# Performance work log

Measured on AMD Instinct MI355X. Metric: run time of the kernel, lower is better.

## Reference

```python
import jax, jax.numpy as jnp
import numpy as np

N, E, DIN, DH, DOUT, H, G = 50000, 640000, 128, 64, 64, 4, 16

_PARAM_SHAPES = {
    "gat1_W": (DIN, H * DH), "gat1_asrc": (H, DH), "gat1_adst": (H, DH), "gat1_b": (DH,),
    "gat2_W": (DH, H * DH), "gat2_asrc": (H, DH), "gat2_adst": (H, DH), "gat2_b": (DH,),
    "gin_W1": (DH, DH), "gin_b1": (DH,), "gin_W2": (DH, DH), "gin_b2": (DH,),
    "sage1_Wl": (DH, DH), "sage1_bl": (DH,), "sage1_Wr": (DH, DH),
    "sage2_Wl": (DH, DH), "sage2_bl": (DH,), "sage2_Wr": (DH, DH),
    "tr_Wq": (DH, H * DH), "tr_bq": (H * DH,), "tr_Wk": (DH, H * DH), "tr_bk": (H * DH,),
    "tr_Wv": (DH, H * DH), "tr_bv": (H * DH,), "tr_Ws": (DH, DH), "tr_bs": (DH,),
    "ec_W1": (2 * DH, DH), "ec_b1": (DH,), "ec_W2": (DH, DH), "ec_b2": (DH,),
    "fc1_W": (DH, DH), "fc1_b": (DH,), "fc2_W": (DH, DOUT), "fc2_b": (DOUT,),
}
_PARAM_NAMES = list(_PARAM_SHAPES)


def setup_inputs() -> dict:
    key = jax.random.key(0)
    inp = {}
    inp["x"] = jax.random.normal(jax.random.fold_in(key, 0), (N, DIN), jnp.float32)
    inp["edge_index"] = jax.random.randint(jax.random.fold_in(key, 1), (2, E), 0, N, dtype=jnp.int32)
    inp["batch"] = jnp.sort(jax.random.randint(jax.random.fold_in(key, 2), (N,), 0, G, dtype=jnp.int32))
    for i, (name, shp) in enumerate(_PARAM_SHAPES.items()):
        inp[name] = jax.random.normal(jax.random.fold_in(key, 10 + i), shp, jnp.float32) * 0.05
    return inp


def _edge_softmax(logit, dst, n):
    # softmax over incoming edges of each target node (PyG scatter-softmax)
    m = jax.ops.segment_max(logit, dst, num_segments=n)
    e = jnp.exp(logit - m[dst])
    z = jax.ops.segment_sum(e, dst, num_segments=n)
    return e / (z[dst] + 1e-16)


def _forward(x, src, dst, batch, p):
    relu = jax.nn.relu
    # GATConv adds self-loops by default
    loop = jnp.arange(N, dtype=src.dtype)
    src_sl = jnp.concatenate([src, loop])
    dst_sl = jnp.concatenate([dst, loop])

    def gat(h_in, W, a_s, a_d, b):
        h = (h_in @ W).reshape(N, H, DH)                    # [N,H,D]
        ls = jnp.einsum('nhd,hd->nh', h, a_s)
        ld = jnp.einsum('nhd,hd->nh', h, a_d)
        logit = jax.nn.leaky_relu(ls[src_sl] + ld[dst_sl], 0.2)   # [E+N,H]
        alpha = _edge_softmax(logit, dst_sl, N)
        out = jax.ops.segment_sum(h[src_sl] * alpha[:, :, None], dst_sl, num_segments=N)
        return out.mean(axis=1) + b                          # concat=False -> head mean + bias

    x1 = relu(gat(x, p["gat1_W"], p["gat1_asrc"], p["gat1_adst"], p["gat1_b"]))
    x2 = relu(gat(x1, p["gat2_W"], p["gat2_asrc"], p["gat2_adst"], p["gat2_b"]))

    # GINConv: nn((1+eps)*x + sum_j x_j), eps=0
    agg = jax.ops.segment_sum(x2[src], dst, num_segments=N)
    x3 = relu(relu((x2 + agg) @ p["gin_W1"] + p["gin_b1"]) @ p["gin_W2"] + p["gin_b2"])

    deg = jax.ops.segment_sum(jnp.ones((E,), x.dtype), dst, num_segments=N)
    deg = jnp.maximum(deg, 1.0)[:, None]

    def sage(h_in, Wl, bl, Wr):
        mean = jax.ops.segment_sum(h_in[src], dst, num_segments=N) / deg
        return mean @ Wl + bl + h_in @ Wr

    xs = relu(sage(x3, p["sage1_Wl"], p["sage1_bl"], p["sage1_Wr"]))
    x4 = relu(sage(xs, p["sage2_Wl"], p["sage2_bl"], p["sage2_Wr"]))

    # TransformerConv (heads=4, concat=False, root_weight skip)
    q = (x4 @ p["tr_Wq"] + p["tr_bq"]).reshape(N, H, DH)
    k = (x4 @ p["tr_Wk"] + p["tr_bk"]).reshape(N, H, DH)
    v = (x4 @ p["tr_Wv"] + p["tr_bv"]).reshape(N, H, DH)
    logit = (q[dst] * k[src]).sum(-1) * (1.0 / np.sqrt(DH))  # [E,H]
    alpha = _edge_softmax(logit, dst, N)
    tout = jax.ops.segment_sum(v[src] * alpha[:, :, None], dst, num_segments=N).mean(axis=1)
    x5 = relu(tout + x4 @ p["tr_Ws"] + p["tr_bs"])

    # EdgeConv: max_j nn([x_i, x_j - x_i])
    xi = x5[dst]
    feat = jnp.concatenate([xi, x5[src] - xi], axis=1)       # [E, 2*DH]
    msg = relu(feat @ p["ec_W1"] + p["ec_b1"]) @ p["ec_W2"] + p["ec_b2"]
    emax = jax.ops.segment_max(msg, dst, num_segments=N)
    x6 = relu(jnp.where(jnp.isfinite(emax), emax, 0.0))      # isolated nodes -> 0

    # global_mean_pool over batch ids
    cnt = jax.ops.segment_sum(jnp.ones((N,), x.dtype), batch, num_segments=G)
    gmean = jax.ops.segment_sum(x6, batch, num_segments=G) / jnp.maximum(cnt, 1.0)[:, None]

    # dropout layers are identity in eval mode
    return relu(gmean @ p["fc1_W"] + p["fc1_b"]) @ p["fc2_W"] + p["fc2_b"]


def reference(x, edge_index, batch,
              gat1_W, gat1_asrc, gat1_adst, gat1_b,
              gat2_W, gat2_asrc, gat2_adst, gat2_b,
              gin_W1, gin_b1, gin_W2, gin_b2,
              sage1_Wl, sage1_bl, sage1_Wr,
              sage2_Wl, sage2_bl, sage2_Wr,
              tr_Wq, tr_bq, tr_Wk, tr_bk, tr_Wv, tr_bv, tr_Ws, tr_bs,
              ec_W1, ec_b1, ec_W2, ec_b2,
              fc1_W, fc1_b, fc2_W, fc2_b):
    L = dict(locals())
    p = {n: L[n] for n in _PARAM_NAMES}
    return _forward(x, edge_index[0], edge_index[1], batch, p)
```

## Files before the change

kernel.cpp:

```cpp
#include <hip/hip_runtime.h>

#define NN 50000
#define EE 640000
#define GG 16
#define N64 (NN*64)

static inline int cdiv(int a,int b){return (a+b-1)/b;}

typedef __attribute__((ext_vector_type(8))) short bfrag;
typedef __attribute__((ext_vector_type(4))) float ffrag;

__device__ __forceinline__ float lrelu(float x){ return x>0.f? x : 0.2f*x; }
__device__ __forceinline__ unsigned fenc(float f){
  unsigned u=__float_as_uint(f);
  return (u&0x80000000u)? ~u : (u|0x80000000u);
}
__device__ __forceinline__ float bf2f(unsigned short u){ return __uint_as_float(((unsigned)u)<<16); }
__device__ __forceinline__ unsigned short f2bf(float f){
  unsigned u=__float_as_uint(f);
  u += 0x7FFFu + ((u>>16)&1u);
  return (unsigned short)(u>>16);
}
__device__ __forceinline__ void mac4(float* acc, const float4 av,
    const float4 w0, const float4 w1, const float4 w2, const float4 w3){
  acc[0]+=av.x*w0.x+av.y*w1.x+av.z*w2.x+av.w*w3.x;
  acc[1]+=av.x*w0.y+av.y*w1.y+av.z*w2.y+av.w*w3.y;
  acc[2]+=av.x*w0.z+av.y*w1.z+av.z*w2.z+av.w*w3.z;
  acc[3]+=av.x*w0.w+av.y*w1.w+av.z*w2.w+av.w*w3.w;
}

__global__ void zero_kernel(unsigned* p, int n){
  int i=blockIdx.x*blockDim.x+threadIdx.x;
  if(i<n) p[i]=0u;
}

__global__ void hist_kernel(const int* __restrict__ dst, int* __restrict__ cnt){
  int e=blockIdx.x*blockDim.x+threadIdx.x;
  if(e<EE) atomicAdd(&cnt[dst[e]],1);
}

__global__ __launch_bounds__(1024) void scan1_kernel(const int* __restrict__ cnt,
    int* __restrict__ rowptr, int* __restrict__ bsum){
  __shared__ int wsum[16];
  int t=threadIdx.x, b=blockIdx.x;
  int i=b*1024+t;
  int v=(i<NN)?cnt[i]:0;
  int lane=t&63, w=t>>6;
  int inc=v;
  #pragma unroll
  for(int o=1;o<64;o<<=1){ int u=__shfl_up(inc,o,64); if(lane>=o) inc+=u; }
  if(lane==63) wsum[w]=inc;
  __syncthreads();
  if(t<16){
    int s=wsum[t];
    #pragma unroll
    for(int o=1;o<16;o<<=1){ int u=__shfl_up(s,o,16); if(t>=o) s+=u; }
    wsum[t]=s;
  }
  __syncthreads();
  int woff=(w>0)?wsum[w-1]:0;
  if(i<NN) rowptr[i]=woff+inc-v;
  if(t==1023) bsum[b]=wsum[15];
}

__global__ void scan2_kernel(const int* __restrict__ bsum, int* __restrict__ boff, int* __restrict__ rowptr, int nb){
  int t=threadIdx.x;
  int v=(t<nb)?bsum[t]:0;
  int inc=v;
  #pragma unroll
  for(int o=1;o<64;o<<=1){ int u=__shfl_up(inc,o,64); if(t>=o) inc+=u; }
  if(t<nb) boff[t]=inc-v;
  if(t==63) rowptr[NN]=inc;
}

__global__ void scan3_kernel(int* __restrict__ rowptr, const int* __restrict__ boff,
                             const int* __restrict__ cnt, float* __restrict__ invdeg){
  int i=blockIdx.x*blockDim.x+threadIdx.x;
  if(i<NN){
    rowptr[i]+=boff[i>>10];
    invdeg[i]=1.f/fmaxf((float)cnt[i],1.f);
  }
}

__global__ void fill_kernel(const int* __restrict__ src, const int* __restrict__ dst,
                            const int* __restrict__ rowptr, int* __restrict__ fillp,
                            int* __restrict__ srcS, int* __restrict__ dstS){
  int e=blockIdx.x*blockDim.x+threadIdx.x;
  if(e>=EE) return;
  int d=dst[e];
  int p=rowptr[d]+atomicAdd(&fillp[d],1);
  srcS[p]=src[e]; dstS[p]=d;
}

__global__ void cvtx_kernel(const float* __restrict__ x, unsigned short* __restrict__ xb){
  int i=blockIdx.x*blockDim.x+threadIdx.x;
  if(i>=NN*32) return;
  float4 v=*(const float4*)(x+(size_t)i*4);
  ushort4 o; o.x=f2bf(v.x); o.y=f2bf(v.y); o.z=f2bf(v.z); o.w=f2bf(v.w);
  *(ushort4*)(xb+(size_t)i*4)=o;
}

__global__ void prep_kernel(
    const float* __restrict__ g1W, const float* __restrict__ g2W,
    const float* __restrict__ giW1, const float* __restrict__ giW2,
    const float* __restrict__ s1Wl, const float* __restrict__ s1Wr,
    const float* __restrict__ s2Wl, const float* __restrict__ s2Wr,
    const float* __restrict__ Wq, const float* __restrict__ Wk,
    const float* __restrict__ Wv, const float* __restrict__ Ws,
    const float* __restrict__ ecW1,
    const float* __restrict__ bq, const float* __restrict__ bk, const float* __restrict__ eb1,
    unsigned short* __restrict__ wt, float* __restrict__ bqk, float* __restrict__ bPQ){
  int i=blockIdx.x*blockDim.x+threadIdx.x;
  if(i<32768){ int n=i>>7,k=i&127; wt[i]=f2bf(g1W[k*256+n]); return; } i-=32768;
  if(i<16384){ int n=i>>6,k=i&63; wt[32768+i]=f2bf(g2W[k*256+n]); return; } i-=16384;
  if(i<4096){ int n=i>>6,k=i&63; wt[49152+i]=f2bf(giW1[k*64+n]); return; } i-=4096;
  if(i<4096){ int n=i>>6,k=i&63; wt[53248+i]=f2bf(giW2[k*64+n]); return; } i-=4096;
  if(i<8192){ int n=i>>7,k=i&127; float v=(k<64)?s1Wl[k*64+n]:s1Wr[(k-64)*64+n];
              wt[57344+i]=f2bf(v); return; } i-=8192;
  if(i<8192){ int n=i>>7,k=i&127; float v=(k<64)?s2Wl[k*64+n]:s2Wr[(k-64)*64+n];
              wt[65536+i]=f2bf(v); return; } i-=8192;
  if(i<32768){ int n=i>>6,k=i&63; float v=(n<256)?Wq[k*256+n]:Wk[k*256+(n-256)];
               wt[73728+i]=f2bf(v); return; } i-=32768;
  if(i<16384){ int n=i>>6,k=i&63; wt[106496+i]=f2bf(Wv[k*256+n]); return; } i-=16384;
  if(i<4096){ int n=i>>6,k=i&63; wt[122880+i]=f2bf(Ws[k*64+n]); return; } i-=4096;
  if(i<8192){ int n=i>>6,k=i&63;
              float v=(n<64)?(ecW1[k*64+n]-ecW1[(64+k)*64+n]):ecW1[(64+k)*64+(n-64)];
              wt[126976+i]=f2bf(v); return; } i-=8192;
  if(i<640){
    if(i<256) bqk[i]=bq[i];
    else if(i<512) bqk[i]=bk[i-256];
    else { int j=i-512; bPQ[j]=(j<64)?eb1[j]:0.f; }
  }
}

template<int K>
__global__ __launch_bounds__(256) void mgemm_kernel(
    const unsigned short* __restrict__ A, const unsigned short* __restrict__ Wt,
    const float* __restrict__ bias,
    float* __restrict__ Cf, unsigned short* __restrict__ Cb, int ldc, int relu_flag,
    const float* __restrict__ a_s, const float* __restrict__ a_d,
    float* __restrict__ lsO, float* __restrict__ ldO){
  __shared__ float lsP[2][4][64];
  const int m0=blockIdx.x*64;
  const int tid=threadIdx.x;
  const int w=tid>>6, l=tid&63, lo=l&15, quad=l>>4;
  const int colg=blockIdx.y*64 + w*16 + lo;
  const unsigned short* wrow=Wt+(size_t)colg*K+quad*8;
  ffrag acc[4];
  #pragma unroll
  for(int t=0;t<4;t++) acc[t]=(ffrag){0.f,0.f,0.f,0.f};
  int rows[4];
  #pragma unroll
  for(int t=0;t<4;t++){ int r=m0+t*16+lo; rows[t]=(r<NN)?r:(NN-1); }
  #pragma unroll
  for(int kc=0;kc<K;kc+=32){
    bfrag b=*(const bfrag*)(wrow+kc);
    #pragma unroll
    for(int t=0;t<4;t++){
      bfrag a=*(const bfrag*)(A+(size_t)rows[t]*K+kc+quad*8);
      acc[t]=__builtin_amdgcn_mfma_f32_16x16x32_bf16(a,b,acc[t],0,0,0);
    }
  }
  float bv=bias?bias[colg]:0.f;
  float asv=0.f,adv=0.f;
  if(lsO){ asv=a_s[colg]; adv=a_d[colg]; }
  #pragma unroll
  for(int t=0;t<4;t++){
    #pragma unroll
    for(int r=0;r<4;r++){
      float v=acc[t][r]+bv;
      if(relu_flag) v=fmaxf(v,0.f);
      int row=m0+t*16+quad*4+r;
      if(row<NN){
        if(Cb) Cb[(size_t)row*ldc+colg]=f2bf(v);
        else   Cf[(size_t)row*ldc+colg]=v;
      }
      if(lsO){
        float ps=v*asv, pd=v*adv;
        #pragma unroll
        for(int o=1;o<16;o<<=1){ ps+=__shfl_xor(ps,o,16); pd+=__shfl_xor(pd,o,16); }
        if(lo==0){ int lr=t*16+quad*4+r; lsP[0][w][lr]=ps; lsP[1][w][lr]=pd; }
      }
    }
  }
  if(lsO){
    __syncthreads();
    if(tid<64){
      int row=m0+tid;
      if(row<NN){
        lsO[(size_t)row*4+blockIdx.y]=lsP[0][0][tid]+lsP[0][1][tid]+lsP[0][2][tid]+lsP[0][3][tid];
        ldO[(size_t)row*4+blockIdx.y]=lsP[1][0][tid]+lsP[1][1][tid]+lsP[1][2][tid]+lsP[1][3][tid];
      }
    }
  }
}

__global__ __launch_bounds__(256) void gat1p_kernel(const unsigned short* __restrict__ h,
    const int* __restrict__ rowptr, const int* __restrict__ srcS,
    const float* __restrict__ ls4, const float* __restrict__ ld4,
    const float* __restrict__ bias, unsigned short* __restrict__ outb){
  int n=blockIdx.x*4+(threadIdx.x>>6);
  int lane=threadIdx.x&63;
  if(n>=NN) return;
  int r0=rowptr[n], r1=rowptr[n+1];
  const float4 ldv=*(const float4*)(ld4+(size_t)4*n);
  const float4 lsv=*(const float4*)(ls4+(size_t)4*n);
  float z0=__expf(lrelu(lsv.x+ldv.x)), z1=__expf(lrelu(lsv.y+ldv.y));
  float z2=__expf(lrelu(lsv.z+ldv.z)), z3=__expf(lrelu(lsv.w+ldv.w));
  const unsigned short* hn=h+(size_t)n*256;
  float a0=z0*bf2f(hn[lane]), a1=z1*bf2f(hn[64+lane]), a2=z2*bf2f(hn[128+lane]), a3=z3*bf2f(hn[192+lane]);
  int j=r0;
  for(; j+3<r1; j+=4){
    int s0=srcS[j], s1=srcS[j+1], s2=srcS[j+2], s3=srcS[j+3];
    const float4 A0=*(const float4*)(ls4+(size_t)4*s0);
    const float4 A1=*(const float4*)(ls4+(size_t)4*s1);
    const float4 A2=*(const float4*)(ls4+(size_t)4*s2);
    const float4 A3=*(const float4*)(ls4+(size_t)4*s3);
    const unsigned short* h0=h+(size_t)s0*256;
    const unsigned short* h1=h+(size_t)s1*256;
    const unsigned short* h2=h+(size_t)s2*256;
    const unsigned short* h3=h+(size_t)s3*256;
    float e00=__expf(lrelu(A0.x+ldv.x)), e01=__expf(lrelu(A0.y+ldv.y));
    float e02=__expf(lrelu(A0.z+ldv.z)), e03=__expf(lrelu(A0.w+ldv.w));
    float e10=__expf(lrelu(A1.x+ldv.x)), e11=__expf(lrelu(A1.y+ldv.y));
    float e12=__expf(lrelu(A1.z+ldv.z)), e13=__expf(lrelu(A1.w+ldv.w));
    float e20=__expf(lrelu(A2.x+ldv.x)), e21=__expf(lrelu(A2.y+ldv.y));
    float e22=__expf(lrelu(A2.z+ldv.z)), e23=__expf(lrelu(A2.w+ldv.w));
    float e30=__expf(lrelu(A3.x+ldv.x)), e31=__expf(lrelu(A3.y+ldv.y));
    float e32=__expf(lrelu(A3.z+ldv.z)), e33=__expf(lrelu(A3.w+ldv.w));
    z0+=(e00+e10)+(e20+e30); z1+=(e01+e11)+(e21+e31);
    z2+=(e02+e12)+(e22+e32); z3+=(e03+e13)+(e23+e33);
    a0+=(e00*bf2f(h0[lane])+e10*bf2f(h1[lane]))+(e20*bf2f(h2[lane])+e30*bf2f(h3[lane]));
    a1+=(e01*bf2f(h0[64+lane])+e11*bf2f(h1[64+lane]))+(e21*bf2f(h2[64+lane])+e31*bf2f(h3[64+lane]));
    a2+=(e02*bf2f(h0[128+lane])+e12*bf2f(h1[128+lane]))+(e22*bf2f(h2[128+lane])+e32*bf2f(h3[128+lane]));
    a3+=(e03*bf2f(h0[192+lane])+e13*bf2f(h1[192+lane]))+(e23*bf2f(h2[192+lane])+e33*bf2f(h3[192+lane]));
  }
  for(; j<r1; j++){
    int s0=srcS[j];
    const float4 A0=*(const float4*)(ls4+(size_t)4*s0);
    const unsigned short* h0=h+(size_t)s0*256;
    float e00=__expf(lrelu(A0.x+ldv.x)), e01=__expf(lrelu(A0.y+ldv.y));
    float e02=__expf(lrelu(A0.z+ldv.z)), e03=__expf(lrelu(A0.w+ldv.w));
    z0+=e00; z1+=e01; z2+=e02; z3+=e03;
    a0+=e00*bf2f(h0[lane]); a1+=e01*bf2f(h0[64+lane]); a2+=e02*bf2f(h0[128+lane]); a3+=e03*bf2f(h0[192+lane]);
  }
  float zi0=1.f/(z0+1e-16f), zi1=1.f/(z1+1e-16f), zi2=1.f/(z2+1e-16f), zi3=1.f/(z3+1e-16f);
  float r=fmaxf(0.25f*(a0*zi0+a1*zi1+a2*zi2+a3*zi3)+bias[lane],0.f);
  outb[(size_t)n*64+lane]=f2bf(r);
}

__global__ __launch_bounds__(256) void agg_kernel(const unsigned short* __restrict__ xin,
    const int* __restrict__ rowptr, const int* __restrict__ srcS,
    unsigned short* __restrict__ out){
  int n=blockIdx.x*4+(threadIdx.x>>6);
  int lane=threadIdx.x&63;
  if(n>=NN) return;
  int r0=rowptr[n], r1=rowptr[n+1];
  float acc=bf2f(xin[(size_t)n*64+lane]);
  int j=r0;
  for(; j+3<r1; j+=4){
    int s0=srcS[j], s1=srcS[j+1], s2=srcS[j+2], s3=srcS[j+3];
    acc+=(bf2f(xin[(size_t)s0*64+lane])+bf2f(xin[(size_t)s1*64+lane]))
        +(bf2f(xin[(size_t)s2*64+lane])+bf2f(xin[(size_t)s3*64+lane]));
  }
  for(; j<r1; j++) acc+=bf2f(xin[(size_t)srcS[j]*64+lane]);
  out[(size_t)n*64+lane]=f2bf(acc);
}

__global__ __launch_bounds__(256) void agg2_kernel(const unsigned short* __restrict__ xin,
    const int* __restrict__ rowptr, const int* __restrict__ srcS,
    const float* __restrict__ invdeg, unsigned short* __restrict__ out128b){
  int n=blockIdx.x*4+(threadIdx.x>>6);
  int lane=threadIdx.x&63;
  if(n>=NN) return;
  int r0=rowptr[n], r1=rowptr[n+1];
  float acc=0.f;
  int j=r0;
  for(; j+3<r1; j+=4){
    int s0=srcS[j], s1=srcS[j+1], s2=srcS[j+2], s3=srcS[j+3];
    acc+=(bf2f(xin[(size_t)s0*64+lane])+bf2f(xin[(size_t)s1*64+lane]))
        +(bf2f(xin[(size_t)s2*64+lane])+bf2f(xin[(size_t)s3*64+lane]));
  }
  for(; j<r1; j++) acc+=bf2f(xin[(size_t)srcS[j]*64+lane]);
  out128b[(size_t)n*128+lane]=f2bf(acc*invdeg[n]);
  out128b[(size_t)n*128+64+lane]=xin[(size_t)n*64+lane];
}

__global__ __launch_bounds__(256) void tr_pass1_kernel(const int* __restrict__ srcS, const int* __restrict__ dstS,
    const unsigned short* __restrict__ qk, float* __restrict__ lg){
  int e=blockIdx.x*16+(threadIdx.x>>4);
  int t=threadIdx.x&15;
  if(e>=EE) return;
  int s=srcS[e], d=dstS[e];
  const unsigned short* qd=qk+(size_t)d*512+t*4;
  const unsigned short* ks=qk+(size_t)s*512+256+t*4;
  ushort4 ku0=*(const ushort4*)(ks);
  ushort4 ku1=*(const ushort4*)(ks+64);
  ushort4 ku2=*(const ushort4*)(ks+128);
  ushort4 ku3=*(const ushort4*)(ks+192);
  ushort4 qu0=*(const ushort4*)(qd);
  ushort4 qu1=*(const ushort4*)(qd+64);
  ushort4 qu2=*(const ushort4*)(qd+128);
  ushort4 qu3=*(const ushort4*)(qd+192);
  float v0=bf2f(ku0.x)*bf2f(qu0.x)+bf2f(ku0.y)*bf2f(qu0.y)+bf2f(ku0.z)*bf2f(qu0.z)+bf2f(ku0.w)*bf2f(qu0.w);
  float v1=bf2f(ku1.x)*bf2f(qu1.x)+bf2f(ku1.y)*bf2f(qu1.y)+bf2f(ku1.z)*bf2f(qu1.z)+bf2f(ku1.w)*bf2f(qu1.w);
  float v2=bf2f(ku2.x)*bf2f(qu2.x)+bf2f(ku2.y)*bf2f(qu2.y)+bf2f(ku2.z)*bf2f(qu2.z)+bf2f(ku2.w)*bf2f(qu2.w);
  float v3=bf2f(ku3.x)*bf2f(qu3.x)+bf2f(ku3.y)*bf2f(qu3.y)+bf2f(ku3.z)*bf2f(qu3.z)+bf2f(ku3.w)*bf2f(qu3.w);
  #pragma unroll
  for(int o=1;o<16;o<<=1){
    v0+=__shfl_xor(v0,o,16); v1+=__shfl_xor(v1,o,16);
    v2+=__shfl_xor(v2,o,16); v3+=__shfl_xor(v3,o,16);
  }
  if(t==0)
    *(float4*)(lg+(size_t)4*e)=make_float4(v0*0.125f,v1*0.125f,v2*0.125f,v3*0.125f);
}

__global__ __launch_bounds__(256) void tr_pass2_kernel(const int* __restrict__ rowptr, const int* __restrict__ srcS,
    const float* __restrict__ lg,
    const unsigned short* __restrict__ v, const float* __restrict__ skip, unsigned short* __restrict__ x5b){
  int n=blockIdx.x*4+(threadIdx.x>>6);
  int lane=threadIdx.x&63;
  if(n>=NN) return;
  int r0=rowptr[n], r1=rowptr[n+1];
  float z0=0.f,z1=0.f,z2=0.f,z3=0.f;
  float a0=0.f,a1=0.f,a2=0.f,a3=0.f;
  int j=r0;
  for(; j+3<r1; j+=4){
    int s0=srcS[j], s1=srcS[j+1], s2=srcS[j+2], s3=srcS[j+3];
    const float4 f0=*(const float4*)(lg+(size_t)4*j);
    const float4 f1=*(const float4*)(lg+(size_t)4*(j+1));
    const float4 f2=*(const float4*)(lg+(size_t)4*(j+2));
    const float4 f3=*(const float4*)(lg+(size_t)4*(j+3));
    const unsigned short* v0=v+(size_t)s0*256;
    const unsigned short* v1=v+(size_t)s1*256;
    const unsigned short* v2=v+(size_t)s2*256;
    const unsigned short* v3=v+(size_t)s3*256;
    float e00=__expf(f0.x), e01=__expf(f0.y), e02=__expf(f0.z), e03=__expf(f0.w);
    float e10=__expf(f1.x), e11=__expf(f1.y), e12=__expf(f1.z), e13=__expf(f1.w);
    float e20=__expf(f2.x), e21=__expf(f2.y), e22=__expf(f2.z), e23=__expf(f2.w);
    float e30=__expf(f3.x), e31=__expf(f3.y), e32=__expf(f3.z), e33=__expf(f3.w);
    z0+=(e00+e10)+(e20+e30); z1+=(e01+e11)+(e21+e31);
    z2+=(e02+e12)+(e22+e32); z3+=(e03+e13)+(e23+e33);
    a0+=(e00*bf2f(v0[lane])+e10*bf2f(v1[lane]))+(e20*bf2f(v2[lane])+e30*bf2f(v3[lane]));
    a1+=(e01*bf2f(v0[64+lane])+e11*bf2f(v1[64+lane]))+(e21*bf2f(v2[64+lane])+e31*bf2f(v3[64+lane]));
    a2+=(e02*bf2f(v0[128+lane])+e12*bf2f(v1[128+lane]))+(e22*bf2f(v2[128+lane])+e32*bf2f(v3[128+lane]));
    a3+=(e03*bf2f(v0[192+lane])+e13*bf2f(v1[192+lane]))+(e23*bf2f(v2[192+lane])+e33*bf2f(v3[192+lane]));
  }
  for(; j<r1; j++){
    int s0=srcS[j];
    const float4 f0=*(const float4*)(lg+(size_t)4*j);
    const unsigned short* v0=v+(size_t)s0*256;
    float e00=__expf(f0.x), e01=__expf(f0.y), e02=__expf(f0.z), e03=__expf(f0.w);
    z0+=e00; z1+=e01; z2+=e02; z3+=e03;
    a0+=e00*bf2f(v0[lane]); a1+=e01*bf2f(v0[64+lane]); a2+=e02*bf2f(v0[128+lane]); a3+=e03*bf2f(v0[192+lane]);
  }
  float zi0=1.f/(z0+1e-16f), zi1=1.f/(z1+1e-16f), zi2=1.f/(z2+1e-16f), zi3=1.f/(z3+1e-16f);
  float t=0.25f*(a0*zi0+a1*zi1+a2*zi2+a3*zi3)+skip[(size_t)n*64+lane];
  x5b[(size_t)n*64+lane]=f2bf(fmaxf(t,0.f));
}

__global__ __launch_bounds__(256) void edgeconv2_kernel(
    const float* __restrict__ PQ,
    const int* __restrict__ srcS, const int* __restrict__ dstS,
    const float* __restrict__ W2, const float* __restrict__ b2,
    unsigned* __restrict__ emax){
  __shared__ float As[64][68];
  __shared__ float Ws[64][64];
  __shared__ int dstL[64];
  const int e0=blockIdx.x*64;
  const int tid=threadIdx.x, tx=tid&15, ty=tid>>4;
  if(tid<64) dstL[tid]=dstS[e0+tid];
  #pragma unroll
  for(int it=0;it<4;it++){
    int linear=it*1024+tid*4;
    int m=linear>>6, k=linear&63;
    int e=e0+m;
    int dn=dstS[e], sn=srcS[e];
    const float4 p=*(const float4*)(PQ+(size_t)dn*128+k);
    const float4 q=*(const float4*)(PQ+(size_t)sn*128+64+k);
    float4 v=make_float4(fmaxf(p.x+q.x,0.f),fmaxf(p.y+q.y,0.f),fmaxf(p.z+q.z,0.f),fmaxf(p.w+q.w,0.f));
    *(float4*)&As[m][k]=v;
  }
  #pragma unroll
  for(int it=0;it<4;it++){
    int linear=it*1024+tid*4;
    int k=linear>>6, n=linear&63;
    *(float4*)&Ws[k][n]=*(const float4*)(W2+(size_t)k*64+n);
  }
  __syncthreads();
  float acc2[4][4];
  #pragma unroll
  for(int i=0;i<4;i++)
    #pragma unroll
    for(int j=0;j<4;j++) acc2[i][j]=b2[tx*4+j];
  #pragma unroll 8
  for(int k=0;k<64;k+=4){
    float4 a0=*(float4*)&As[ty*4+0][k];
    float4 a1=*(float4*)&As[ty*4+1][k];
    float4 a2=*(float4*)&As[ty*4+2][k];
    float4 a3=*(float4*)&As[ty*4+3][k];
    float4 w0=*(float4*)&Ws[k+0][tx*4];
    float4 w1=*(float4*)&Ws[k+1][tx*4];
    float4 w2=*(float4*)&Ws[k+2][tx*4];
    float4 w3=*(float4*)&Ws[k+3][tx*4];
    mac4(acc2[0],a0,w0,w1,w2,w3);
    mac4(acc2[1],a1,w0,w1,w2,w3);
    mac4(acc2[2],a2,w0,w1,w2,w3);
    mac4(acc2[3],a3,w0,w1,w2,w3);
  }
  __syncthreads();
  #pragma unroll
  for(int i=0;i<4;i++)
    #pragma unroll
    for(int j=0;j<4;j++)
      As[ty*4+i][tx*4+j]=acc2[i][j];
  __syncthreads();
  if(tid<64){
    const int c=tid;
    const int dFirst=dstL[0], dLast=dstL[63];
    int dprev=dFirst;
    float mx=As[0][c];
    #pragma unroll 8
    for(int m=1;m<64;m++){
      int dn=dstL[m];
      float v=As[m][c];
      if(dn!=dprev){
        unsigned* addr=&emax[(size_t)dprev*64+c];
        unsigned enc=fenc(mx);
        if(dprev!=dFirst && dprev!=dLast) *addr=enc;
        else atomicMax(addr,enc);
        dprev=dn; mx=v;
      }else mx=fmaxf(mx,v);
    }
    unsigned* addr=&emax[(size_t)dprev*64+c];
    unsigned enc=fenc(mx);
    if(dprev!=dFirst && dprev!=dLast) *addr=enc;
    else atomicMax(addr,enc);
  }
}

__global__ __launch_bounds__(256) void pool_kernel(const unsigned* __restrict__ emax, const int* __restrict__ batch,
                                                   float* __restrict__ pooled){
  const int NB=200;
  int base=blockIdx.x*NB;
  int lane=threadIdx.x&63;
  int wsub=threadIdx.x>>6;
  float acc=0.f; int curg=-1;
  for(int idx=wsub; idx<NB; idx+=4){
    int n=base+idx;
    if(n>=NN) break;
    int g=batch[n];
    if(g!=curg){
      if(curg>=0) atomicAdd(&pooled[curg*64+lane],acc);
      acc=0.f; curg=g;
    }
    unsigned u=emax[(size_t)n*64+lane];
    acc+=(u>=0x80000000u)? __uint_as_float(u&0x7fffffffu) : 0.f;
  }
  if(curg>=0) atomicAdd(&pooled[curg*64+lane],acc);
}

__global__ __launch_bounds__(256) void final_kernel(const float* __restrict__ pooled, const int* __restrict__ batch,
    const float* __restrict__ fc1W, const float* __restrict__ fc1b,
    const float* __restrict__ fc2W, const float* __restrict__ fc2b,
    float* __restrict__ out){
  __shared__ float gm[16][64];
  __shared__ float t1[16][64];
  __shared__ int cgs[17];
// ... 33 lines not shown
  const int*   src     =ei;
  const int*   dst     =ei+EE;
  const int*   batch   =(const int*)  d_in[2];
  const float* gat1_W  =(const float*)d_in[3];
  const float* gat1_as =(const float*)d_in[4];
  const float* gat1_ad =(const float*)d_in[5];
  const float* gat1_b  =(const float*)d_in[6];
  const float* gat2_W  =(const float*)d_in[7];
  const float* gat2_as =(const float*)d_in[8];
  const float* gat2_ad =(const float*)d_in[9];
  const float* gat2_b  =(const float*)d_in[10];
  const float* gin_W1  =(const float*)d_in[11];
  const float* gin_b1  =(const float*)d_in[12];
  const float* gin_W2  =(const float*)d_in[13];
  const float* gin_b2  =(const float*)d_in[14];
  const float* sage1_Wl=(const float*)d_in[15];
  const float* sage1_bl=(const float*)d_in[16];
  const float* sage1_Wr=(const float*)d_in[17];
  const float* sage2_Wl=(const float*)d_in[18];
  const float* sage2_bl=(const float*)d_in[19];
  const float* sage2_Wr=(const float*)d_in[20];
  const float* tr_Wq   =(const float*)d_in[21];
  const float* tr_bq   =(const float*)d_in[22];
  const float* tr_Wk   =(const float*)d_in[23];
  const float* tr_bk   =(const float*)d_in[24];
  const float* tr_Wv   =(const float*)d_in[25];
  const float* tr_bv   =(const float*)d_in[26];
  const float* tr_Ws   =(const float*)d_in[27];
  const float* tr_bs   =(const float*)d_in[28];
  const float* ec_W1   =(const float*)d_in[29];
  const float* ec_b1   =(const float*)d_in[30];
  const float* ec_W2   =(const float*)d_in[31];
  const float* ec_b2   =(const float*)d_in[32];
  const float* fc1_W   =(const float*)d_in[33];
  const float* fc1_b   =(const float*)d_in[34];
  const float* fc2_W   =(const float*)d_in[35];
  const float* fc2_b   =(const float*)d_in[36];

  float* base=(float*)d_ws;
  size_t off=0;
  auto alloc=[&](size_t n){ float* p=base+off; off+=n; return p; };
  float* A_big =alloc((size_t)NN*256);
  float* nb0   =alloc(N64);
  float* nb1   =alloc(N64);
  float* nb2   =alloc(N64);
  float* nb3   =alloc(N64);
  float* nb4   =alloc(N64);
  float* nb5   =alloc(N64);
  float* logitE=alloc((size_t)EE*4);
  float* ls    =alloc(NN*4);
  float* ldb   =alloc(NN*4);
  float* invdeg=alloc(NN);
  float* pooled=alloc(GG*64);
  float* wbuf  =alloc(68000);
  float* bbuf  =alloc(640);
  int* ibase=(int*)(base+off);
  int* srcS  =ibase;
  int* dstS  =ibase+EE;
  int* cnt   =ibase+2*EE;
  int* fillp =ibase+2*EE+NN;
  int* rowptr=ibase+2*EE+2*NN;
  int* bsum  =ibase+2*EE+3*NN+8;
  int* boff  =bsum+64;

  const int BT=256;
  const int NSB=cdiv(NN,1024);
  zero_kernel<<<cdiv(2*NN,BT),BT,0,stream>>>((unsigned*)cnt,2*NN);
  zero_kernel<<<cdiv(GG*64,BT),BT,0,stream>>>((unsigned*)pooled,GG*64);
  zero_kernel<<<cdiv(N64,BT),BT,0,stream>>>((unsigned*)nb5,N64);
  hist_kernel<<<cdiv(EE,BT),BT,0,stream>>>(dst,cnt);
  scan1_kernel<<<NSB,1024,0,stream>>>(cnt,rowptr,bsum);
  scan2_kernel<<<1,64,0,stream>>>(bsum,boff,rowptr,NSB);
  scan3_kernel<<<cdiv(NN,BT),BT,0,stream>>>(rowptr,boff,cnt,invdeg);
  fill_kernel<<<cdiv(EE,BT),BT,0,stream>>>(src,dst,rowptr,fillp,srcS,dstS);

  const int GB=cdiv(NN,64);
  const int GW=cdiv(NN,4);

  unsigned short* wt =(unsigned short*)wbuf;
  float* bqk=bbuf;
  float* bPQ=bbuf+512;
  unsigned short* hbf  =(unsigned short*)A_big;
  unsigned short* xb   =(unsigned short*)A_big+(size_t)NN*256;
  unsigned short* xcatb=(unsigned short*)A_big;
  unsigned short* qkb  =(unsigned short*)A_big;
  unsigned short* x1b  =(unsigned short*)nb0;
  unsigned short* x2b  =(unsigned short*)nb1;
  unsigned short* tb   =(unsigned short*)nb2;
  unsigned short* hb3  =(unsigned short*)nb3;
  unsigned short* x3b  =(unsigned short*)nb1;
  unsigned short* xsb  =(unsigned short*)nb2;
  unsigned short* x4b  =(unsigned short*)nb0;
  unsigned short* vb   =(unsigned short*)nb1;
  unsigned short* x5b  =(unsigned short*)nb4;
  float* skipf=nb3;
  float* PQf  =nb1;

  prep_kernel<<<cdiv(135808,BT),BT,0,stream>>>(gat1_W,gat2_W,gin_W1,gin_W2,
      sage1_Wl,sage1_Wr,sage2_Wl,sage2_Wr,tr_Wq,tr_Wk,tr_Wv,tr_Ws,ec_W1,
      tr_bq,tr_bk,ec_b1,wt,bqk,bPQ);
  cvtx_kernel<<<cdiv(NN*32,BT),BT,0,stream>>>(x,xb);

  mgemm_kernel<128><<<dim3(GB,4),BT,0,stream>>>(xb,wt,nullptr,nullptr,hbf,256,0,
                                                gat1_as,gat1_ad,ls,ldb);
  gat1p_kernel<<<GW,BT,0,stream>>>(hbf,rowptr,srcS,ls,ldb,gat1_b,x1b);
  mgemm_kernel<64><<<dim3(GB,4),BT,0,stream>>>(x1b,wt+32768,nullptr,nullptr,hbf,256,0,
                                               gat2_as,gat2_ad,ls,ldb);
  gat1p_kernel<<<GW,BT,0,stream>>>(hbf,rowptr,srcS,ls,ldb,gat2_b,x2b);
  agg_kernel<<<GW,BT,0,stream>>>(x2b,rowptr,srcS,tb);
  mgemm_kernel<64><<<dim3(GB,1),BT,0,stream>>>(tb,wt+49152,gin_b1,nullptr,hb3,64,1,
                                               nullptr,nullptr,nullptr,nullptr);
  mgemm_kernel<64><<<dim3(GB,1),BT,0,stream>>>(hb3,wt+53248,gin_b2,nullptr,x3b,64,1,
                                               nullptr,nullptr,nullptr,nullptr);
  agg2_kernel<<<GW,BT,0,stream>>>(x3b,rowptr,srcS,invdeg,xcatb);
  mgemm_kernel<128><<<dim3(GB,1),BT,0,stream>>>(xcatb,wt+57344,sage1_bl,nullptr,xsb,64,1,
                                                nullptr,nullptr,nullptr,nullptr);
  agg2_kernel<<<GW,BT,0,stream>>>(xsb,rowptr,srcS,invdeg,xcatb);
  mgemm_kernel<128><<<dim3(GB,1),BT,0,stream>>>(xcatb,wt+65536,sage2_bl,nullptr,x4b,64,1,
                                                nullptr,nullptr,nullptr,nullptr);
  mgemm_kernel<64><<<dim3(GB,8),BT,0,stream>>>(x4b,wt+73728,bqk,nullptr,qkb,512,0,
                                               nullptr,nullptr,nullptr,nullptr);
  tr_pass1_kernel<<<cdiv(EE,16),BT,0,stream>>>(srcS,dstS,qkb,logitE);
  mgemm_kernel<64><<<dim3(GB,4),BT,0,stream>>>(x4b,wt+106496,tr_bv,nullptr,vb,256,0,
                                               nullptr,nullptr,nullptr,nullptr);
  mgemm_kernel<64><<<dim3(GB,1),BT,0,stream>>>(x4b,wt+122880,tr_bs,skipf,nullptr,64,0,
                                               nullptr,nullptr,nullptr,nullptr);
  tr_pass2_kernel<<<GW,BT,0,stream>>>(rowptr,srcS,logitE,vb,skipf,x5b);
  mgemm_kernel<64><<<dim3(GB,2),BT,0,stream>>>(x5b,wt+126976,bPQ,PQf,nullptr,128,0,
                                               nullptr,nullptr,nullptr,nullptr);
  edgeconv2_kernel<<<EE/64,BT,0,stream>>>(PQf,srcS,dstS,ec_W2,ec_b2,(unsigned*)nb5);
  pool_kernel<<<cdiv(NN,200),BT,0,stream>>>((unsigned*)nb5,batch,pooled);
  final_kernel<<<1,BT,0,stream>>>(pooled,batch,fc1_W,fc1_b,fc2_W,fc2_b,(float*)d_out);
}
```

Measured before the change: 879.4 us.

## Split GAT/transformer aggregation across two waves per node; MFMA bf16 edgeconv

The GAT and transformer aggregation kernels now give each node two wavefronts, each handling half of its incoming edges, and combine the partial sums through shared memory. This is meant to expose more memory-level parallelism for the gathers. The edgeconv second layer now uses bf16 MFMA instructions with a pre-transposed bf16 W2, in place of a scalar fp32 tiled GEMM. The PQ intermediate is stored as bf16 rather than fp32, halving its gather traffic. The costs are an extra block barrier and shared-memory reduction per node pair, plus reduced precision in the edge MLP.

```diff
diff --git a/kernel.cpp b/kernel.cpp
--- a/kernel.cpp
+++ b/kernel.cpp
@@ -20,13 +20,6 @@
   unsigned u=__float_as_uint(f);
   u += 0x7FFFu + ((u>>16)&1u);
   return (unsigned short)(u>>16);
-}
-__device__ __forceinline__ void mac4(float* acc, const float4 av,
-    const float4 w0, const float4 w1, const float4 w2, const float4 w3){
-  acc[0]+=av.x*w0.x+av.y*w1.x+av.z*w2.x+av.w*w3.x;
-  acc[1]+=av.x*w0.y+av.y*w1.y+av.z*w2.y+av.w*w3.y;
-  acc[2]+=av.x*w0.z+av.y*w1.z+av.z*w2.z+av.w*w3.z;
-  acc[3]+=av.x*w0.w+av.y*w1.w+av.z*w2.w+av.w*w3.w;
 }
 
 __global__ void zero_kernel(unsigned* p, int n){
@@ -107,7 +100,7 @@
     const float* __restrict__ s2Wl, const float* __restrict__ s2Wr,
     const float* __restrict__ Wq, const float* __restrict__ Wk,
     const float* __restrict__ Wv, const float* __restrict__ Ws,
-    const float* __restrict__ ecW1,
+    const float* __restrict__ ecW1, const float* __restrict__ ecW2,
     const float* __restrict__ bq, const float* __restrict__ bk, const float* __restrict__ eb1,
     unsigned short* __restrict__ wt, float* __restrict__ bqk, float* __restrict__ bPQ){
   int i=blockIdx.x*blockDim.x+threadIdx.x;
@@ -126,6 +119,7 @@
   if(i<8192){ int n=i>>6,k=i&63;
               float v=(n<64)?(ecW1[k*64+n]-ecW1[(64+k)*64+n]):ecW1[(64+k)*64+(n-64)];
               wt[126976+i]=f2bf(v); return; } i-=8192;
+  if(i<4096){ int n=i>>6,k=i&63; wt[135168+i]=f2bf(ecW2[k*64+n]); return; } i-=4096;
   if(i<640){
     if(i<256) bqk[i]=bq[i];
     else if(i<512) bqk[i]=bk[i-256];
@@ -199,54 +193,79 @@
     const int* __restrict__ rowptr, const int* __restrict__ srcS,
     const float* __restrict__ ls4, const float* __restrict__ ld4,
     const float* __restrict__ bias, unsigned short* __restrict__ outb){
-  int n=blockIdx.x*4+(threadIdx.x>>6);
-  int lane=threadIdx.x&63;
-  if(n>=NN) return;
-  int r0=rowptr[n], r1=rowptr[n+1];
-  const float4 ldv=*(const float4*)(ld4+(size_t)4*n);
-  const float4 lsv=*(const float4*)(ls4+(size_t)4*n);
-  float z0=__expf(lrelu(lsv.x+ldv.x)), z1=__expf(lrelu(lsv.y+ldv.y));
-  float z2=__expf(lrelu(lsv.z+ldv.z)), z3=__expf(lrelu(lsv.w+ldv.w));
-  const unsigned short* hn=h+(size_t)n*256;
-  float a0=z0*bf2f(hn[lane]), a1=z1*bf2f(hn[64+lane]), a2=z2*bf2f(hn[128+lane]), a3=z3*bf2f(hn[192+lane]);
-  int j=r0;
-  for(; j+3<r1; j+=4){
-    int s0=srcS[j], s1=srcS[j+1], s2=srcS[j+2], s3=srcS[j+3];
-    const float4 A0=*(const float4*)(ls4+(size_t)4*s0);
-    const float4 A1=*(const float4*)(ls4+(size_t)4*s1);
-    const float4 A2=*(const float4*)(ls4+(size_t)4*s2);
-    const float4 A3=*(const float4*)(ls4+(size_t)4*s3);
-    const unsigned short* h0=h+(size_t)s0*256;
-    const unsigned short* h1=h+(size_t)s1*256;
-    const unsigned short* h2=h+(size_t)s2*256;
-    const unsigned short* h3=h+(size_t)s3*256;
-    float e00=__expf(lrelu(A0.x+ldv.x)), e01=__expf(lrelu(A0.y+ldv.y));
-    float e02=__expf(lrelu(A0.z+ldv.z)), e03=__expf(lrelu(A0.w+ldv.w));
-    float e10=__expf(lrelu(A1.x+ldv.x)), e11=__expf(lrelu(A1.y+ldv.y));
-    float e12=__expf(lrelu(A1.z+ldv.z)), e13=__expf(lrelu(A1.w+ldv.w));
-    float e20=__expf(lrelu(A2.x+ldv.x)), e21=__expf(lrelu(A2.y+ldv.y));
-    float e22=__expf(lrelu(A2.z+ldv.z)), e23=__expf(lrelu(A2.w+ldv.w));
-    float e30=__expf(lrelu(A3.x+ldv.x)), e31=__expf(lrelu(A3.y+ldv.y));
-    float e32=__expf(lrelu(A3.z+ldv.z)), e33=__expf(lrelu(A3.w+ldv.w));
-    z0+=(e00+e10)+(e20+e30); z1+=(e01+e11)+(e21+e31);
-    z2+=(e02+e12)+(e22+e32); z3+=(e03+e13)+(e23+e33);
-    a0+=(e00*bf2f(h0[lane])+e10*bf2f(h1[lane]))+(e20*bf2f(h2[lane])+e30*bf2f(h3[lane]));
-    a1+=(e01*bf2f(h0[64+lane])+e11*bf2f(h1[64+lane]))+(e21*bf2f(h2[64+lane])+e31*bf2f(h3[64+lane]));
-    a2+=(e02*bf2f(h0[128+lane])+e12*bf2f(h1[128+lane]))+(e22*bf2f(h2[128+lane])+e32*bf2f(h3[128+lane]));
-    a3+=(e03*bf2f(h0[192+lane])+e13*bf2f(h1[192+lane]))+(e23*bf2f(h2[192+lane])+e33*bf2f(h3[192+lane]));
-  }
-  for(; j<r1; j++){
-    int s0=srcS[j];
-    const float4 A0=*(const float4*)(ls4+(size_t)4*s0);
-    const unsigned short* h0=h+(size_t)s0*256;
-    float e00=__expf(lrelu(A0.x+ldv.x)), e01=__expf(lrelu(A0.y+ldv.y));
-    float e02=__expf(lrelu(A0.z+ldv.z)), e03=__expf(lrelu(A0.w+ldv.w));
-    z0+=e00; z1+=e01; z2+=e02; z3+=e03;
-    a0+=e00*bf2f(h0[lane]); a1+=e01*bf2f(h0[64+lane]); a2+=e02*bf2f(h0[128+lane]); a3+=e03*bf2f(h0[192+lane]);
-  }
-  float zi0=1.f/(z0+1e-16f), zi1=1.f/(z1+1e-16f), zi2=1.f/(z2+1e-16f), zi3=1.f/(z3+1e-16f);
-  float r=fmaxf(0.25f*(a0*zi0+a1*zi1+a2*zi2+a3*zi3)+bias[lane],0.f);
-  outb[(size_t)n*64+lane]=f2bf(r);
+  __shared__ float cz[4][4];
+  __shared__ float ca[4][4][64];
+  int w=threadIdx.x>>6, lane=threadIdx.x&63;
+  int n=blockIdx.x*2+(w>>1);
+  int half=w&1;
+  float z0=0.f,z1=0.f,z2=0.f,z3=0.f;
+  float a0=0.f,a1=0.f,a2=0.f,a3=0.f;
+  if(n<NN){
+    int r0=rowptr[n], r1=rowptr[n+1];
+    int mid=(r0+r1)>>1;
+    const float4 ldv=*(const float4*)(ld4+(size_t)4*n);
+    if(half==0){
+      const float4 lsv=*(const float4*)(ls4+(size_t)4*n);
+      z0=__expf(lrelu(lsv.x+ldv.x)); z1=__expf(lrelu(lsv.y+ldv.y));
+      z2=__expf(lrelu(lsv.z+ldv.z)); z3=__expf(lrelu(lsv.w+ldv.w));
+      const unsigned short* hn=h+(size_t)n*256;
+      a0=z0*bf2f(hn[lane]); a1=z1*bf2f(hn[64+lane]);
+      a2=z2*bf2f(hn[128+lane]); a3=z3*bf2f(hn[192+lane]);
+    }
+    int j = half? mid : r0;
+    int je= half? r1  : mid;
+    for(; j+3<je; j+=4){
+      int s0=srcS[j], s1=srcS[j+1], s2=srcS[j+2], s3=srcS[j+3];
+      const float4 A0=*(const float4*)(ls4+(size_t)4*s0);
+      const float4 A1=*(const float4*)(ls4+(size_t)4*s1);
+      const float4 A2=*(const float4*)(ls4+(size_t)4*s2);
+      const float4 A3=*(const float4*)(ls4+(size_t)4*s3);
+      const unsigned short* h0=h+(size_t)s0*256;
+      const unsigned short* h1=h+(size_t)s1*256;
+      const unsigned short* h2=h+(size_t)s2*256;
+      const unsigned short* h3=h+(size_t)s3*256;
+      float e00=__expf(lrelu(A0.x+ldv.x)), e01=__expf(lrelu(A0.y+ldv.y));
+      float e02=__expf(lrelu(A0.z+ldv.z)), e03=__expf(lrelu(A0.w+ldv.w));
+      float e10=__expf(lrelu(A1.x+ldv.x)), e11=__expf(lrelu(A1.y+ldv.y));
+      float e12=__expf(lrelu(A1.z+ldv.z)), e13=__expf(lrelu(A1.w+ldv.w));
+      float e20=__expf(lrelu(A2.x+ldv.x)), e21=__expf(lrelu(A2.y+ldv.y));
+      float e22=__expf(lrelu(A2.z+ldv.z)), e23=__expf(lrelu(A2.w+ldv.w));
+      float e30=__expf(lrelu(A3.x+ldv.x)), e31=__expf(lrelu(A3.y+ldv.y));
+      float e32=__expf(lrelu(A3.z+ldv.z)), e33=__expf(lrelu(A3.w+ldv.w));
+      z0+=(e00+e10)+(e20+e30); z1+=(e01+e11)+(e21+e31);
+      z2+=(e02+e12)+(e22+e32); z3+=(e03+e13)+(e23+e33);
+      a0+=(e00*bf2f(h0[lane])+e10*bf2f(h1[lane]))+(e20*bf2f(h2[lane])+e30*bf2f(h3[lane]));
+      a1+=(e01*bf2f(h0[64+lane])+e11*bf2f(h1[64+lane]))+(e21*bf2f(h2[64+lane])+e31*bf2f(h3[64+lane]));
+      a2+=(e02*bf2f(h0[128+lane])+e12*bf2f(h1[128+lane]))+(e22*bf2f(h2[128+lane])+e32*bf2f(h3[128+lane]));
+      a3+=(e03*bf2f(h0[192+lane])+e13*bf2f(h1[192+lane]))+(e23*bf2f(h2[192+lane])+e33*bf2f(h3[192+lane]));
+    }
+    for(; j<je; j++){
+      int s0=srcS[j];
+      const float4 A0=*(const float4*)(ls4+(size_t)4*s0);
+      const unsigned short* h0=h+(size_t)s0*256;
+      float e00=__expf(lrelu(A0.x+ldv.x)), e01=__expf(lrelu(A0.y+ldv.y));
+      float e02=__expf(lrelu(A0.z+ldv.z)), e03=__expf(lrelu(A0.w+ldv.w));
+      z0+=e00; z1+=e01; z2+=e02; z3+=e03;
+      a0+=e00*bf2f(h0[lane]); a1+=e01*bf2f(h0[64+lane]);
+      a2+=e02*bf2f(h0[128+lane]); a3+=e03*bf2f(h0[192+lane]);
+    }
+  }
+  if(lane==0){ cz[w][0]=z0; cz[w][1]=z1; cz[w][2]=z2; cz[w][3]=z3; }
+  ca[w][0][lane]=a0; ca[w][1][lane]=a1; ca[w][2][lane]=a2; ca[w][3][lane]=a3;
+  __syncthreads();
+  if(threadIdx.x<128){
+    int ni=threadIdx.x>>6, l=threadIdx.x&63;
+    int n2=blockIdx.x*2+ni;
+    if(n2<NN){
+      int w0=ni*2, w1=w0+1;
+      float Z0=cz[w0][0]+cz[w1][0], Z1=cz[w0][1]+cz[w1][1];
+      float Z2=cz[w0][2]+cz[w1][2], Z3=cz[w0][3]+cz[w1][3];
+      float A0=ca[w0][0][l]+ca[w1][0][l], A1=ca[w0][1][l]+ca[w1][1][l];
+      float A2=ca[w0][2][l]+ca[w1][2][l], A3=ca[w0][3][l]+ca[w1][3][l];
+      float r=0.25f*(A0/(Z0+1e-16f)+A1/(Z1+1e-16f)+A2/(Z2+1e-16f)+A3/(Z3+1e-16f))+bias[l];
+      outb[(size_t)n2*64+l]=f2bf(fmaxf(r,0.f));
+    }
+  }
 }
 
 __global__ __launch_bounds__(256) void agg_kernel(const unsigned short* __restrict__ xin,
@@ -318,57 +337,77 @@
 __global__ __launch_bounds__(256) void tr_pass2_kernel(const int* __restrict__ rowptr, const int* __restrict__ srcS,
     const float* __restrict__ lg,
     const unsigned short* __restrict__ v, const float* __restrict__ skip, unsigned short* __restrict__ x5b){
-  int n=blockIdx.x*4+(threadIdx.x>>6);
-  int lane=threadIdx.x&63;
-  if(n>=NN) return;
-  int r0=rowptr[n], r1=rowptr[n+1];
+  __shared__ float cz[4][4];
+  __shared__ float ca[4][4][64];
+  int w=threadIdx.x>>6, lane=threadIdx.x&63;
+  int n=blockIdx.x*2+(w>>1);
+  int half=w&1;
   float z0=0.f,z1=0.f,z2=0.f,z3=0.f;
   float a0=0.f,a1=0.f,a2=0.f,a3=0.f;
-  int j=r0;
-  for(; j+3<r1; j+=4){
-    int s0=srcS[j], s1=srcS[j+1], s2=srcS[j+2], s3=srcS[j+3];
-    const float4 f0=*(const float4*)(lg+(size_t)4*j);
-    const float4 f1=*(const float4*)(lg+(size_t)4*(j+1));
-    const float4 f2=*(const float4*)(lg+(size_t)4*(j+2));
-    const float4 f3=*(const float4*)(lg+(size_t)4*(j+3));
-    const unsigned short* v0=v+(size_t)s0*256;
-    const unsigned short* v1=v+(size_t)s1*256;
-    const unsigned short* v2=v+(size_t)s2*256;
-    const unsigned short* v3=v+(size_t)s3*256;
-    float e00=__expf(f0.x), e01=__expf(f0.y), e02=__expf(f0.z), e03=__expf(f0.w);
-    float e10=__expf(f1.x), e11=__expf(f1.y), e12=__expf(f1.z), e13=__expf(f1.w);
-    float e20=__expf(f2.x), e21=__expf(f2.y), e22=__expf(f2.z), e23=__expf(f2.w);
-    float e30=__expf(f3.x), e31=__expf(f3.y), e32=__expf(f3.z), e33=__expf(f3.w);
-    z0+=(e00+e10)+(e20+e30); z1+=(e01+e11)+(e21+e31);
-    z2+=(e02+e12)+(e22+e32); z3+=(e03+e13)+(e23+e33);
-    a0+=(e00*bf2f(v0[lane])+e10*bf2f(v1[lane]))+(e20*bf2f(v2[lane])+e30*bf2f(v3[lane]));
-    a1+=(e01*bf2f(v0[64+lane])+e11*bf2f(v1[64+lane]))+(e21*bf2f(v2[64+lane])+e31*bf2f(v3[64+lane]));
-    a2+=(e02*bf2f(v0[128+lane])+e12*bf2f(v1[128+lane]))+(e22*bf2f(v2[128+lane])+e32*bf2f(v3[128+lane]));
-    a3+=(e03*bf2f(v0[192+lane])+e13*bf2f(v1[192+lane]))+(e23*bf2f(v2[192+lane])+e33*bf2f(v3[192+lane]));
-  }
-  for(; j<r1; j++){
-    int s0=srcS[j];
-    const float4 f0=*(const float4*)(lg+(size_t)4*j);
-    const unsigned short* v0=v+(size_t)s0*256;
-    float e00=__expf(f0.x), e01=__expf(f0.y), e02=__expf(f0.z), e03=__expf(f0.w);
-    z0+=e00; z1+=e01; z2+=e02; z3+=e03;
-    a0+=e00*bf2f(v0[lane]); a1+=e01*bf2f(v0[64+lane]); a2+=e02*bf2f(v0[128+lane]); a3+=e03*bf2f(v0[192+lane]);
-  }
-  float zi0=1.f/(z0+1e-16f), zi1=1.f/(z1+1e-16f), zi2=1.f/(z2+1e-16f), zi3=1.f/(z3+1e-16f);
-  float t=0.25f*(a0*zi0+a1*zi1+a2*zi2+a3*zi3)+skip[(size_t)n*64+lane];
-  x5b[(size_t)n*64+lane]=f2bf(fmaxf(t,0.f));
-}
-
-__global__ __launch_bounds__(256) void edgeconv2_kernel(
-    const float* __restrict__ PQ,
+  if(n<NN){
+    int r0=rowptr[n], r1=rowptr[n+1];
+    int mid=(r0+r1)>>1;
+    int j = half? mid : r0;
+    int je= half? r1  : mid;
+    for(; j+3<je; j+=4){
+      int s0=srcS[j], s1=srcS[j+1], s2=srcS[j+2], s3=srcS[j+3];
+      const float4 f0=*(const float4*)(lg+(size_t)4*j);
+      const float4 f1=*(const float4*)(lg+(size_t)4*(j+1));
+      const float4 f2=*(const float4*)(lg+(size_t)4*(j+2));
+      const float4 f3=*(const float4*)(lg+(size_t)4*(j+3));
+      const unsigned short* v0=v+(size_t)s0*256;
+      const unsigned short* v1=v+(size_t)s1*256;
+      const unsigned short* v2=v+(size_t)s2*256;
+      const unsigned short* v3=v+(size_t)s3*256;
+      float e00=__expf(f0.x), e01=__expf(f0.y), e02=__expf(f0.z), e03=__expf(f0.w);
+      float e10=__expf(f1.x), e11=__expf(f1.y), e12=__expf(f1.z), e13=__expf(f1.w);
+      float e20=__expf(f2.x), e21=__expf(f2.y), e22=__expf(f2.z), e23=__expf(f2.w);
+      float e30=__expf(f3.x), e31=__expf(f3.y), e32=__expf(f3.z), e33=__expf(f3.w);
+      z0+=(e00+e10)+(e20+e30); z1+=(e01+e11)+(e21+e31);
+      z2+=(e02+e12)+(e22+e32); z3+=(e03+e13)+(e23+e33);
+      a0+=(e00*bf2f(v0[lane])+e10*bf2f(v1[lane]))+(e20*bf2f(v2[lane])+e30*bf2f(v3[lane]));
+      a1+=(e01*bf2f(v0[64+lane])+e11*bf2f(v1[64+lane]))+(e21*bf2f(v2[64+lane])+e31*bf2f(v3[64+lane]));
+      a2+=(e02*bf2f(v0[128+lane])+e12*bf2f(v1[128+lane]))+(e22*bf2f(v2[128+lane])+e32*bf2f(v3[128+lane]));
+      a3+=(e03*bf2f(v0[192+lane])+e13*bf2f(v1[192+lane]))+(e23*bf2f(v2[192+lane])+e33*bf2f(v3[192+lane]));
+    }
+    for(; j<je; j++){
+      int s0=srcS[j];
+      const float4 f0=*(const float4*)(lg+(size_t)4*j);
+      const unsigned short* v0=v+(size_t)s0*256;
+      float e00=__expf(f0.x), e01=__expf(f0.y), e02=__expf(f0.z), e03=__expf(f0.w);
+      z0+=e00; z1+=e01; z2+=e02; z3+=e03;
+      a0+=e00*bf2f(v0[lane]); a1+=e01*bf2f(v0[64+lane]);
+      a2+=e02*bf2f(v0[128+lane]); a3+=e03*bf2f(v0[192+lane]);
+    }
+  }
+  if(lane==0){ cz[w][0]=z0; cz[w][1]=z1; cz[w][2]=z2; cz[w][3]=z3; }
+  ca[w][0][lane]=a0; ca[w][1][lane]=a1; ca[w][2][lane]=a2; ca[w][3][lane]=a3;
+  __syncthreads();
+  if(threadIdx.x<128){
+    int ni=threadIdx.x>>6, l=threadIdx.x&63;
+    int n2=blockIdx.x*2+ni;
+    if(n2<NN){
+      int w0=ni*2, w1=w0+1;
+      float Z0=cz[w0][0]+cz[w1][0], Z1=cz[w0][1]+cz[w1][1];
+      float Z2=cz[w0][2]+cz[w1][2], Z3=cz[w0][3]+cz[w1][3];
+      float A0=ca[w0][0][l]+ca[w1][0][l], A1=ca[w0][1][l]+ca[w1][1][l];
+      float A2=ca[w0][2][l]+ca[w1][2][l], A3=ca[w0][3][l]+ca[w1][3][l];
+      float t=0.25f*(A0/(Z0+1e-16f)+A1/(Z1+1e-16f)+A2/(Z2+1e-16f)+A3/(Z3+1e-16f))+skip[(size_t)n2*64+l];
+      x5b[(size_t)n2*64+l]=f2bf(fmaxf(t,0.f));
+    }
+  }
+}
+
+__global__ __launch_bounds__(256) void edgeconv3_kernel(
+    const unsigned short* __restrict__ PQ,
     const int* __restrict__ srcS, const int* __restrict__ dstS,
-    const float* __restrict__ W2, const float* __restrict__ b2,
+    const unsigned short* __restrict__ W2t, const float* __restrict__ b2,
     unsigned* __restrict__ emax){
-  __shared__ float As[64][68];
-  __shared__ float Ws[64][64];
+  __shared__ unsigned short Hs[64][72];
+  __shared__ float As[64][66];
   __shared__ int dstL[64];
   const int e0=blockIdx.x*64;
-  const int tid=threadIdx.x, tx=tid&15, ty=tid>>4;
+  const int tid=threadIdx.x;
   if(tid<64) dstL[tid]=dstS[e0+tid];
   #pragma unroll
   for(int it=0;it<4;it++){
@@ -376,44 +415,36 @@
     int m=linear>>6, k=linear&63;
     int e=e0+m;
     int dn=dstS[e], sn=srcS[e];
-    const float4 p=*(const float4*)(PQ+(size_t)dn*128+k);
-    const float4 q=*(const float4*)(PQ+(size_t)sn*128+64+k);
-    float4 v=make_float4(fmaxf(p.x+q.x,0.f),fmaxf(p.y+q.y,0.f),fmaxf(p.z+q.z,0.f),fmaxf(p.w+q.w,0.f));
-    *(float4*)&As[m][k]=v;
-  }
-  #pragma unroll
-  for(int it=0;it<4;it++){
-    int linear=it*1024+tid*4;
-    int k=linear>>6, n=linear&63;
-    *(float4*)&Ws[k][n]=*(const float4*)(W2+(size_t)k*64+n);
-  }
-  __syncthreads();
-  float acc2[4][4];
-  #pragma unroll
-  for(int i=0;i<4;i++)
+    ushort4 pu=*(const ushort4*)(PQ+(size_t)dn*128+k);
+    ushort4 qu=*(const ushort4*)(PQ+(size_t)sn*128+64+k);
+    ushort4 hh;
+    hh.x=f2bf(fmaxf(bf2f(pu.x)+bf2f(qu.x),0.f));
+    hh.y=f2bf(fmaxf(bf2f(pu.y)+bf2f(qu.y),0.f));
+    hh.z=f2bf(fmaxf(bf2f(pu.z)+bf2f(qu.z),0.f));
+    hh.w=f2bf(fmaxf(bf2f(pu.w)+bf2f(qu.w),0.f));
+    *(ushort4*)&Hs[m][k]=hh;
+  }
+  __syncthreads();
+  const int w=tid>>6, l=tid&63, lo=l&15, quad=l>>4;
+  const int colg=w*16+lo;
+  ffrag acc[4];
+  #pragma unroll
+  for(int t=0;t<4;t++) acc[t]=(ffrag){0.f,0.f,0.f,0.f};
+  #pragma unroll
+  for(int kc=0;kc<64;kc+=32){
+    bfrag b=*(const bfrag*)(W2t+(size_t)colg*64+kc+quad*8);
     #pragma unroll
-    for(int j=0;j<4;j++) acc2[i][j]=b2[tx*4+j];
-  #pragma unroll 8
-  for(int k=0;k<64;k+=4){
-    float4 a0=*(float4*)&As[ty*4+0][k];
-    float4 a1=*(float4*)&As[ty*4+1][k];
-    float4 a2=*(float4*)&As[ty*4+2][k];
-    float4 a3=*(float4*)&As[ty*4+3][k];
-    float4 w0=*(float4*)&Ws[k+0][tx*4];
-    float4 w1=*(float4*)&Ws[k+1][tx*4];
-    float4 w2=*(float4*)&Ws[k+2][tx*4];
-    float4 w3=*(float4*)&Ws[k+3][tx*4];
-    mac4(acc2[0],a0,w0,w1,w2,w3);
-    mac4(acc2[1],a1,w0,w1,w2,w3);
-    mac4(acc2[2],a2,w0,w1,w2,w3);
-    mac4(acc2[3],a3,w0,w1,w2,w3);
-  }
-  __syncthreads();
-  #pragma unroll
-  for(int i=0;i<4;i++)
+    for(int t=0;t<4;t++){
+      bfrag a=*(const bfrag*)(&Hs[t*16+lo][kc+quad*8]);
+      acc[t]=__builtin_amdgcn_mfma_f32_16x16x32_bf16(a,b,acc[t],0,0,0);
+    }
+  }
+  float bv=b2[colg];
+  #pragma unroll
+  for(int t=0;t<4;t++)
     #pragma unroll
-    for(int j=0;j<4;j++)
-      As[ty*4+i][tx*4+j]=acc2[i][j];
+    for(int r=0;r<4;r++)
+      As[t*16+quad*4+r][colg]=acc[t][r]+bv;
   __syncthreads();
   if(tid<64){
     const int c=tid;
@@ -553,7 +584,7 @@
   float* ldb   =alloc(NN*4);
   float* invdeg=alloc(NN);
   float* pooled=alloc(GG*64);
-  float* wbuf  =alloc(68000);
+  float* wbuf  =alloc(70000);
   float* bbuf  =alloc(640);
   int* ibase=(int*)(base+off);
   int* srcS  =ibase;
@@ -577,6 +608,7 @@
 
   const int GB=cdiv(NN,64);
   const int GW=cdiv(NN,4);
+  const int GW2=cdiv(NN,2);
 
   unsigned short* wt =(unsigned short*)wbuf;
   float* bqk=bbuf;
@@ -595,19 +627,19 @@
   unsigned short* vb   =(unsigned short*)nb1;
   unsigned short* x5b  =(unsigned short*)nb4;
   float* skipf=nb3;
-  float* PQf  =nb1;
-
-  prep_kernel<<<cdiv(135808,BT),BT,0,stream>>>(gat1_W,gat2_W,gin_W1,gin_W2,
-      sage1_Wl,sage1_Wr,sage2_Wl,sage2_Wr,tr_Wq,tr_Wk,tr_Wv,tr_Ws,ec_W1,
+  unsigned short* PQb  =(unsigned short*)nb1;
+
+  prep_kernel<<<cdiv(139904,BT),BT,0,stream>>>(gat1_W,gat2_W,gin_W1,gin_W2,
+      sage1_Wl,sage1_Wr,sage2_Wl,sage2_Wr,tr_Wq,tr_Wk,tr_Wv,tr_Ws,ec_W1,ec_W2,
       tr_bq,tr_bk,ec_b1,wt,bqk,bPQ);
   cvtx_kernel<<<cdiv(NN*32,BT),BT,0,stream>>>(x,xb);
 
   mgemm_kernel<128><<<dim3(GB,4),BT,0,stream>>>(xb,wt,nullptr,nullptr,hbf,256,0,
                                                 gat1_as,gat1_ad,ls,ldb);
-  gat1p_kernel<<<GW,BT,0,stream>>>(hbf,rowptr,srcS,ls,ldb,gat1_b,x1b);
+  gat1p_kernel<<<GW2,BT,0,stream>>>(hbf,rowptr,srcS,ls,ldb,gat1_b,x1b);
   mgemm_kernel<64><<<dim3(GB,4),BT,0,stream>>>(x1b,wt+32768,nullptr,nullptr,hbf,256,0,
                                                gat2_as,gat2_ad,ls,ldb);
-  gat1p_kernel<<<GW,BT,0,stream>>>(hbf,rowptr,srcS,ls,ldb,gat2_b,x2b);
+  gat1p_kernel<<<GW2,BT,0,stream>>>(hbf,rowptr,srcS,ls,ldb,gat2_b,x2b);
   agg_kernel<<<GW,BT,0,stream>>>(x2b,rowptr,srcS,tb);
   mgemm_kernel<64><<<dim3(GB,1),BT,0,stream>>>(tb,wt+49152,gin_b1,nullptr,hb3,64,1,
                                                nullptr,nullptr,nullptr,nullptr);
@@ -626,10 +658,10 @@
                                                nullptr,nullptr,nullptr,nullptr);
   mgemm_kernel<64><<<dim3(GB,1),BT,0,stream>>>(x4b,wt+122880,tr_bs,skipf,nullptr,64,0,
                                                nullptr,nullptr,nullptr,nullptr);
-  tr_pass2_kernel<<<GW,BT,0,stream>>>(rowptr,srcS,logitE,vb,skipf,x5b);
-  mgemm_kernel<64><<<dim3(GB,2),BT,0,stream>>>(x5b,wt+126976,bPQ,PQf,nullptr,128,0,
+  tr_pass2_kernel<<<GW2,BT,0,stream>>>(rowptr,srcS,logitE,vb,skipf,x5b);
+  mgemm_kernel<64><<<dim3(GB,2),BT,0,stream>>>(x5b,wt+126976,bPQ,nullptr,PQb,128,0,
                                                nullptr,nullptr,nullptr,nullptr);
-  edgeconv2_kernel<<<EE/64,BT,0,stream>>>(PQf,srcS,dstS,ec_W2,ec_b2,(unsigned*)nb5);
+  edgeconv3_kernel<<<EE/64,BT,0,stream>>>(PQb,srcS,dstS,wt+135168,ec_b2,(unsigned*)nb5);
   pool_kernel<<<cdiv(NN,200),BT,0,stream>>>((unsigned*)nb5,batch,pooled);
   final_kernel<<<1,BT,0,stream>>>(pooled,batch,fc1_W,fc1_b,fc2_W,fc2_b,(float*)d_out);
 }
```

Result: no change. 865.0 us (-1.6%).
